# Kernel tuning notes

Measured on AMD Instinct MI355X. Metric: run time of the kernel, lower is better.

Reference implementation:

```python
import jax, jax.numpy as jnp
import numpy as np

N_NODES = 100000


def gcn_conv(x, edge_index, W, b):
    """PyG GCNConv: symmetric normalization with added self-loops.
    x: [N, Fin], edge_index: [2, E], W: [Fin, Fout], b: [Fout]
    """
    n = x.shape[0]
    h = x @ W  # [N, Fout] dense transform first (standard GCNConv order)
    loops = jnp.arange(n, dtype=edge_index.dtype)
    src = jnp.concatenate([edge_index[0], loops])  # self-loops appended
    dst = jnp.concatenate([edge_index[1], loops])
    deg = jax.ops.segment_sum(jnp.ones_like(dst, dtype=h.dtype), dst, num_segments=n)
    dinv = jax.lax.rsqrt(deg)  # deg >= 1 thanks to self-loops
    norm = dinv[src] * dinv[dst]  # [E+N]
    msgs = h[src] * norm[:, None]  # gather + scale
    out = jax.ops.segment_sum(msgs, dst, num_segments=n)  # scatter-add
    return out + b


def setup_inputs() -> dict:
    key = jax.random.key(0)
    k = jax.random.split(key, 9)
    in_c, hid, out_c = 128, 128, 64
    n_edges = 1600000
    x = jax.random.normal(k[0], (N_NODES, in_c), dtype=jnp.float32)
    edge_index = jax.random.randint(k[1], (2, n_edges), 0, N_NODES, dtype=jnp.int64)
    def lin(kw, kb, fan_in, fan_out):
        bound = 1.0 / np.sqrt(fan_in)
        W = jax.random.uniform(kw, (fan_in, fan_out), jnp.float32, -bound, bound)
        b = jax.random.uniform(kb, (fan_out,), jnp.float32, -bound, bound)
        return W, b
    W1, b1 = lin(k[2], k[3], in_c, hid)
    W2, b2 = lin(k[4], k[5], hid, hid)
    Wf, bf = lin(k[6], k[7], hid, out_c)
    return {"x": x, "edge_index": edge_index, "W1": W1, "b1": b1,
            "W2": W2, "b2": b2, "Wf": Wf, "bf": bf}


def reference(x, edge_index, W1, b1, W2, b2, Wf, bf):
    h = jax.nn.relu(gcn_conv(x, edge_index, W1, b1))
    h = jax.nn.relu(gcn_conv(h, edge_index, W2, b2))
    return h @ Wf + bf
```

## Files before the change

### kernel.cpp

```cpp
#include <hip/hip_runtime.h>
#include <stdint.h>

typedef short short8 __attribute__((ext_vector_type(8)));
typedef float floatx4 __attribute__((ext_vector_type(4)));

#define BK 256

static __device__ __forceinline__ float bflo(unsigned int u) {
    union { unsigned int i; float f; } v; v.i = u << 16; return v.f;
}
static __device__ __forceinline__ float bfhi(unsigned int u) {
    union { unsigned int i; float f; } v; v.i = u & 0xffff0000u; return v.f;
}
static __device__ __forceinline__ unsigned short f2bf(float f) {
    union { float f; unsigned int i; } v; v.f = f;
    unsigned int u = v.i;
    unsigned int r = u + 0x7fffu + ((u >> 16) & 1u);
    return (unsigned short)(r >> 16);
}


__global__ void k_zero_cnt(int* bucket_cnt, int K) {
    int i = blockIdx.x * 256 + threadIdx.x;
    if (i < K) bucket_cnt[i] = 0;
}

__global__ __launch_bounds__(256) void k_hist(const int* __restrict__ dst, int* bucket_cnt,
                                              int E, int N, int K) {
    __shared__ int h[512];
    int t = threadIdx.x;
    for (int i = t; i < K; i += 256) h[i] = 0;
    __syncthreads();
    int per = (E + gridDim.x - 1) / gridDim.x;
    int lo = blockIdx.x * per, hi = min(lo + per, E);
    for (int e = lo + t; e < hi; e += 256) {
        unsigned int d = (unsigned int)dst[e];
        if (d < (unsigned int)N) atomicAdd(&h[d >> 8], 1);
    }
    __syncthreads();
    for (int i = t; i < K; i += 256) if (h[i]) atomicAdd(&bucket_cnt[i], h[i]);
}

__global__ void k_scanK(const int* __restrict__ bucket_cnt, int* bucket_off, int* bucket_cur,
                        int* row_start, int K, int N) {
    __shared__ int s[512];
    int t = threadIdx.x;
    int v = (t < K) ? bucket_cnt[t] : 0;
    s[t] = v; __syncthreads();
    for (int off = 1; off < 512; off <<= 1) {
        int x = (t >= off) ? s[t - off] : 0;
        __syncthreads();
        s[t] += x;
        __syncthreads();
    }
    if (t < K) { bucket_off[t] = s[t] - v; bucket_cur[t] = s[t] - v; }
    if (t == K - 1) { bucket_off[K] = s[t]; row_start[N] = s[t]; }
}

__global__ __launch_bounds__(256) void k_binscatter(const int* __restrict__ src,
                                                    const int* __restrict__ dst,
                                                    int* bucket_cur, uint2* __restrict__ tmp,
                                                    int E, int N, int K) {
    __shared__ int h[512];
    __shared__ int base[512];
    int t = threadIdx.x;
    for (int i = t; i < K; i += 256) h[i] = 0;
    __syncthreads();
    int per = (E + gridDim.x - 1) / gridDim.x;
    int lo = blockIdx.x * per, hi = min(lo + per, E);
    for (int e = lo + t; e < hi; e += 256) {
        unsigned int d = (unsigned int)dst[e], sv = (unsigned int)src[e];
        if (d < (unsigned int)N && sv < (unsigned int)N) atomicAdd(&h[d >> 8], 1);
    }
    __syncthreads();
    for (int i = t; i < K; i += 256) {
        int c = h[i];
        base[i] = c ? atomicAdd(&bucket_cur[i], c) : 0;
        h[i] = 0;
    }
    __syncthreads();
    for (int e = lo + t; e < hi; e += 256) {
        unsigned int d = (unsigned int)dst[e], sv = (unsigned int)src[e];
        if (d < (unsigned int)N && sv < (unsigned int)N) {
            int k = d >> 8;
            int p = base[k] + atomicAdd(&h[k], 1);
            tmp[p] = make_uint2(sv, d);
        }
    }
}

__global__ __launch_bounds__(256) void k_fine(const uint2* __restrict__ tmp,
                                              const int* __restrict__ bucket_off,
                                              int* __restrict__ row_start, float* __restrict__ dinv,
                                              int* __restrict__ csr, int N) {
    __shared__ int deg[BK];
    __shared__ int scn[BK];
    __shared__ int cur[BK];
    int b = blockIdx.x;
    int t = threadIdx.x;
    int lo = bucket_off[b], hi = bucket_off[b + 1];
    deg[t] = 0;
    __syncthreads();
    for (int e = lo + t; e < hi; e += 256) {
        int d = tmp[e].y & (BK - 1);
        atomicAdd(&deg[d], 1);
    }
    __syncthreads();
    int v = deg[t];
    scn[t] = v; __syncthreads();
    for (int off = 1; off < 256; off <<= 1) {
        int x = (t >= off) ? scn[t - off] : 0;
        __syncthreads();
        scn[t] += x;
        __syncthreads();
    }
    int rs = lo + scn[t] - v;
    cur[t] = rs;
    int node = b * BK + t;
    if (node < N) { row_start[node] = rs; dinv[node] = rsqrtf((float)(v + 1)); }
    __syncthreads();
    for (int e = lo + t; e < hi; e += 256) {
        uint2 ed = tmp[e];
        int d = ed.y & (BK - 1);
        int p = atomicAdd(&cur[d], 1);
        csr[p] = (int)ed.x;
    }
}


template <int NOUT, bool SCALE, bool BIAS, bool XF32, bool OUTF32>
__global__ __launch_bounds__(256, 2) void k_gemm(
    const void* __restrict__ Xv, const float* __restrict__ W,
    const float* __restrict__ bias, const float* __restrict__ dinv,
    void* __restrict__ outv, int M) {
    __shared__ __align__(16) unsigned short Wl[NOUT * 136];
    int t = threadIdx.x;
    for (int idx = t; idx < 128 * NOUT; idx += 256) {
        int k = idx / NOUT, n = idx % NOUT;
        Wl[n * 136 + k] = f2bf(W[idx]);
    }
    __syncthreads();

    int wave = t >> 6, lane = t & 63;
    int quad = lane >> 4, l16 = lane & 15;
    int m0 = blockIdx.x * 64 + wave * 16;
    int mr = m0 + l16;
    int mrc = mr < M ? mr : M - 1;

    constexpr int NT = NOUT / 16;
    floatx4 acc[NT];
#pragma unroll
    for (int i = 0; i < NT; i++) acc[i] = (floatx4){0.f, 0.f, 0.f, 0.f};

#pragma unroll
    for (int kc = 0; kc < 4; kc++) {
        short8 a;
        if (XF32) {
            const float* X = (const float*)Xv;
            const float* p = X + (size_t)mrc * 128 + kc * 32 + quad * 8;
            float4 xa = *(const float4*)p;
            float4 xb = *(const float4*)(p + 4);
            a[0] = (short)f2bf(xa.x); a[1] = (short)f2bf(xa.y);
            a[2] = (short)f2bf(xa.z); a[3] = (short)f2bf(xa.w);
            a[4] = (short)f2bf(xb.x); a[5] = (short)f2bf(xb.y);
            a[6] = (short)f2bf(xb.z); a[7] = (short)f2bf(xb.w);
        } else {
            const unsigned short* X = (const unsigned short*)Xv;
            a = *(const short8*)(X + (size_t)mrc * 128 + kc * 32 + quad * 8);
        }
#pragma unroll
        for (int nt = 0; nt < NT; nt++) {
            short8 b = *(const short8*)(&Wl[(nt * 16 + l16) * 136 + kc * 32 + quad * 8]);
            acc[nt] = __builtin_amdgcn_mfma_f32_16x16x32_bf16(a, b, acc[nt], 0, 0, 0);
        }
    }

#pragma unroll
    for (int i = 0; i < 4; i++) {
        int r = m0 + quad * 4 + i;
        if (r >= M) continue;
        float sc = SCALE ? dinv[r] : 1.0f;
#pragma unroll
        for (int nt = 0; nt < NT; nt++) {
            int n = nt * 16 + l16;
            float v = acc[nt][i] * sc;
            if (BIAS) v += bias[n];
            if (OUTF32) {
                ((float*)outv)[(size_t)r * NOUT + n] = v;
            } else {
                ((unsigned short*)outv)[(size_t)r * NOUT + n] = f2bf(v);
            }
        }
    }
}


__global__ __launch_bounds__(256, 4) void k_aggregate(
    const unsigned short* __restrict__ Hs, const int* __restrict__ csr,
    const int* __restrict__ row_start,
    const float* __restrict__ dinv, const float* __restrict__ bias,
    unsigned short* __restrict__ out, int N, int E) {
    int wave = threadIdx.x >> 6, lane = threadIdx.x & 63;
    int node = blockIdx.x * 4 + wave;
    if (node >= N) return;
    int ch = lane * 2;
    int Nm1 = N - 1;

    unsigned int u = *(const unsigned int*)(Hs + (size_t)node * 128 + ch);
    float a0 = bflo(u), a1 = bfhi(u);

    int start = row_start[node];
    int end = row_start[node + 1];
    if (start < 0) start = 0;
    if (end > E) end = E;
    int e = start;
    for (; e + 4 <= end; e += 4) {
        int s0 = min(max(csr[e], 0), Nm1);
        int s1 = min(max(csr[e + 1], 0), Nm1);
        int s2 = min(max(csr[e + 2], 0), Nm1);
        int s3 = min(max(csr[e + 3], 0), Nm1);
        unsigned int u0 = *(const unsigned int*)(Hs + (size_t)s0 * 128 + ch);
        unsigned int u1 = *(const unsigned int*)(Hs + (size_t)s1 * 128 + ch);
        unsigned int u2 = *(const unsigned int*)(Hs + (size_t)s2 * 128 + ch);
        unsigned int u3 = *(const unsigned int*)(Hs + (size_t)s3 * 128 + ch);
        a0 += bflo(u0) + bflo(u1) + bflo(u2) + bflo(u3);
        a1 += bfhi(u0) + bfhi(u1) + bfhi(u2) + bfhi(u3);
    }
    for (; e < end; e++) {
        int s0 = min(max(csr[e], 0), Nm1);
        unsigned int u0 = *(const unsigned int*)(Hs + (size_t)s0 * 128 + ch);
        a0 += bflo(u0);
        a1 += bfhi(u0);
    }

    float di = dinv[node];
    float r0 = fmaxf(fmaf(di, a0, bias[ch]), 0.f);
    float r1 = fmaxf(fmaf(di, a1, bias[ch + 1]), 0.f);
    unsigned int pk = (unsigned int)f2bf(r0) | ((unsigned int)f2bf(r1) << 16);
    *(unsigned int*)(out + (size_t)node * 128 + ch) = pk;
}


extern "C" void kernel_launch(void* const* d_in, const int* in_sizes, int n_in,
                              void* d_out, int out_size, void* d_ws, size_t ws_size,
                              hipStream_t stream) {
    const float* x  = (const float*)d_in[0];
    const int* ei   = (const int*)d_in[1];
    const float* W1 = (const float*)d_in[2];
    const float* b1 = (const float*)d_in[3];
    const float* W2 = (const float*)d_in[4];
    const float* b2 = (const float*)d_in[5];
    const float* Wf = (const float*)d_in[6];
    const float* bf = (const float*)d_in[7];

    int N = in_sizes[0] / 128;
    int E = in_sizes[1] / 2;
    const int* src = ei;
    const int* dst = ei + E;
    int K = (N + BK - 1) / BK;

    size_t need = 0;
    auto pad = [](size_t b) { return (b + 255) & ~(size_t)255; };
    size_t o_bcnt = need; need += pad(512 * 4);
    size_t o_boff = need; need += pad(513 * 4);
    size_t o_bcur = need; need += pad(512 * 4);
    size_t o_rs   = need; need += pad(((size_t)N + 1) * 4);
    size_t o_dinv = need; need += pad((size_t)N * 4);
    size_t o_csr  = need; need += pad((size_t)E * 4);
    size_t o_hs   = need; need += pad((size_t)N * 128 * 2);
    size_t o_a    = need; need += pad((size_t)N * 128 * 2);
    if (ws_size < need) return;
    if ((size_t)E * 8 > (size_t)N * 128 * 2) return;

    char* ws = (char*)d_ws;
    int* bucket_cnt = (int*)(ws + o_bcnt);
    int* bucket_off = (int*)(ws + o_boff);
    int* bucket_cur = (int*)(ws + o_bcur);
    int* row_start  = (int*)(ws + o_rs);
    float* dinv     = (float*)(ws + o_dinv);
    int* csr        = (int*)(ws + o_csr);
    unsigned short* Hs = (unsigned short*)(ws + o_hs);
    unsigned short* A  = (unsigned short*)(ws + o_a);
    uint2* tmp      = (uint2*)A;

    k_zero_cnt<<<(K + 255) / 256, 256, 0, stream>>>(bucket_cnt, K);
    k_hist<<<256, 256, 0, stream>>>(dst, bucket_cnt, E, N, K);
    k_scanK<<<1, 512, 0, stream>>>(bucket_cnt, bucket_off, bucket_cur, row_start, K, N);
    k_binscatter<<<256, 256, 0, stream>>>(src, dst, bucket_cur, tmp, E, N, K);
    k_fine<<<K, 256, 0, stream>>>(tmp, bucket_off, row_start, dinv, csr, N);

    int GB = (N + 63) / 64;
    k_gemm<128, true, false, true, false><<<GB, 256, 0, stream>>>(x, W1, nullptr, dinv, Hs, N);
    k_aggregate<<<(N + 3) / 4, 256, 0, stream>>>(Hs, csr, row_start, dinv, b1, A, N, E);
    k_gemm<128, true, false, false, false><<<GB, 256, 0, stream>>>(A, W2, nullptr, dinv, Hs, N);
    k_aggregate<<<(N + 3) / 4, 256, 0, stream>>>(Hs, csr, row_start, dinv, b2, A, N, E);
    k_gemm<64, false, true, false, true><<<GB, 256, 0, stream>>>(A, Wf, bf, nullptr, d_out, N);
}
```

Before: 356.6 us.

## Slice feature matrices into 16-channel planes for cache-local gather aggregation

Hidden features are stored as eight 16-channel slices of [N,16] bf16, and aggregation runs one slice per block, so each slice (about 3.2MB) can stay resident in L2 during the random neighbor gathers. Within a wave, eight lanes cooperate on each of eight edges, and the partial sums are combined with cross-lane shuffles. Weights are converted to transposed bf16 once up front instead of in every GEMM block, and the GEMM grid is halved with a grid-stride loop so the weight tile is reused across two row blocks. In exchange there are more blocks, each doing narrower 32-byte gathers, plus extra shuffle reductions per node.

```diff
diff --git a/kernel.cpp b/kernel.cpp
--- a/kernel.cpp
+++ b/kernel.cpp
@@ -128,116 +128,138 @@
 }
 
 
-template <int NOUT, bool SCALE, bool BIAS, bool XF32, bool OUTF32>
+__global__ void k_wconv(const float* __restrict__ W, unsigned short* __restrict__ Wt,
+                        int K, int Nc) {
+    int i = blockIdx.x * 256 + threadIdx.x;
+    if (i < K * Nc) {
+        int k = i / Nc, n = i % Nc;
+        Wt[n * K + k] = f2bf(W[i]);
+    }
+}
+
+
+template <int NOUT, bool SCALE, bool BIAS, bool XF32, bool ASLICED, bool OSLICED>
 __global__ __launch_bounds__(256, 2) void k_gemm(
-    const void* __restrict__ Xv, const float* __restrict__ W,
+    const void* __restrict__ Xv, const unsigned short* __restrict__ Wbf,
     const float* __restrict__ bias, const float* __restrict__ dinv,
-    void* __restrict__ outv, int M) {
+    void* __restrict__ outv, int M, int MB) {
     __shared__ __align__(16) unsigned short Wl[NOUT * 136];
     int t = threadIdx.x;
-    for (int idx = t; idx < 128 * NOUT; idx += 256) {
-        int k = idx / NOUT, n = idx % NOUT;
-        Wl[n * 136 + k] = f2bf(W[idx]);
+    for (int c = t; c < NOUT * 16; c += 256) {
+        short8 v = *(const short8*)(Wbf + (size_t)c * 8);
+        *(short8*)(&Wl[(c >> 4) * 136 + (c & 15) * 8]) = v;
     }
     __syncthreads();
 
     int wave = t >> 6, lane = t & 63;
     int quad = lane >> 4, l16 = lane & 15;
-    int m0 = blockIdx.x * 64 + wave * 16;
-    int mr = m0 + l16;
-    int mrc = mr < M ? mr : M - 1;
-
     constexpr int NT = NOUT / 16;
-    floatx4 acc[NT];
-#pragma unroll
-    for (int i = 0; i < NT; i++) acc[i] = (floatx4){0.f, 0.f, 0.f, 0.f};
-
-#pragma unroll
-    for (int kc = 0; kc < 4; kc++) {
-        short8 a;
-        if (XF32) {
-            const float* X = (const float*)Xv;
-            const float* p = X + (size_t)mrc * 128 + kc * 32 + quad * 8;
-            float4 xa = *(const float4*)p;
-            float4 xb = *(const float4*)(p + 4);
-            a[0] = (short)f2bf(xa.x); a[1] = (short)f2bf(xa.y);
-            a[2] = (short)f2bf(xa.z); a[3] = (short)f2bf(xa.w);
-            a[4] = (short)f2bf(xb.x); a[5] = (short)f2bf(xb.y);
-            a[6] = (short)f2bf(xb.z); a[7] = (short)f2bf(xb.w);
-        } else {
-            const unsigned short* X = (const unsigned short*)Xv;
-            a = *(const short8*)(X + (size_t)mrc * 128 + kc * 32 + quad * 8);
-        }
-#pragma unroll
-        for (int nt = 0; nt < NT; nt++) {
-            short8 b = *(const short8*)(&Wl[(nt * 16 + l16) * 136 + kc * 32 + quad * 8]);
-            acc[nt] = __builtin_amdgcn_mfma_f32_16x16x32_bf16(a, b, acc[nt], 0, 0, 0);
-        }
-    }
-
-#pragma unroll
-    for (int i = 0; i < 4; i++) {
-        int r = m0 + quad * 4 + i;
-        if (r >= M) continue;
-        float sc = SCALE ? dinv[r] : 1.0f;
-#pragma unroll
-        for (int nt = 0; nt < NT; nt++) {
-            int n = nt * 16 + l16;
-            float v = acc[nt][i] * sc;
-            if (BIAS) v += bias[n];
-            if (OUTF32) {
-                ((float*)outv)[(size_t)r * NOUT + n] = v;
+
+    for (int mb = blockIdx.x; mb < MB; mb += gridDim.x) {
+        int m0 = mb * 64 + wave * 16;
+        int mr = m0 + l16;
+        int mrc = mr < M ? mr : M - 1;
+
+        floatx4 acc[NT];
+#pragma unroll
+        for (int i = 0; i < NT; i++) acc[i] = (floatx4){0.f, 0.f, 0.f, 0.f};
+
+#pragma unroll
+        for (int kc = 0; kc < 4; kc++) {
+            short8 a;
+            if (XF32) {
+                const float* X = (const float*)Xv;
+                const float* p = X + (size_t)mrc * 128 + kc * 32 + quad * 8;
+                float4 xa = *(const float4*)p;
+                float4 xb = *(const float4*)(p + 4);
+                a[0] = (short)f2bf(xa.x); a[1] = (short)f2bf(xa.y);
+                a[2] = (short)f2bf(xa.z); a[3] = (short)f2bf(xa.w);
+                a[4] = (short)f2bf(xb.x); a[5] = (short)f2bf(xb.y);
+                a[6] = (short)f2bf(xb.z); a[7] = (short)f2bf(xb.w);
+            } else if (ASLICED) {
+                const unsigned short* X = (const unsigned short*)Xv;
+                int slice = kc * 2 + (quad >> 1);
+                a = *(const short8*)(X + ((size_t)slice * M + mrc) * 16 + (quad & 1) * 8);
             } else {
-                ((unsigned short*)outv)[(size_t)r * NOUT + n] = f2bf(v);
+                const unsigned short* X = (const unsigned short*)Xv;
+                a = *(const short8*)(X + (size_t)mrc * 128 + kc * 32 + quad * 8);
             }
-        }
-    }
-}
-
-
-__global__ __launch_bounds__(256, 4) void k_aggregate(
-    const unsigned short* __restrict__ Hs, const int* __restrict__ csr,
-    const int* __restrict__ row_start,
-    const float* __restrict__ dinv, const float* __restrict__ bias,
-    unsigned short* __restrict__ out, int N, int E) {
+#pragma unroll
+            for (int nt = 0; nt < NT; nt++) {
+                short8 b = *(const short8*)(&Wl[(nt * 16 + l16) * 136 + kc * 32 + quad * 8]);
+                acc[nt] = __builtin_amdgcn_mfma_f32_16x16x32_bf16(a, b, acc[nt], 0, 0, 0);
+            }
+        }
+
+#pragma unroll
+        for (int i = 0; i < 4; i++) {
+            int r = m0 + quad * 4 + i;
+            if (r >= M) continue;
+            float sc = SCALE ? dinv[r] : 1.0f;
+#pragma unroll
+            for (int nt = 0; nt < NT; nt++) {
+                int n = nt * 16 + l16;
+                float v = acc[nt][i] * sc;
+                if (BIAS) v += bias[n];
+                if (OSLICED) {
+                    ((unsigned short*)outv)[((size_t)nt * M + r) * 16 + l16] = f2bf(v);
+                } else {
+                    ((float*)outv)[(size_t)r * NOUT + n] = v;
+                }
+            }
+        }
+    }
+}
+
+
+__global__ __launch_bounds__(256, 8) void k_agg_sliced(
+    const unsigned short* __restrict__ Hst, const int* __restrict__ csr,
+    const int* __restrict__ row_start, const float* __restrict__ dinv,
+    const float* __restrict__ bias, unsigned short* __restrict__ At, int N) {
+    int b = blockIdx.x;
+    int s = b & 7;
+    int nb = b >> 3;
     int wave = threadIdx.x >> 6, lane = threadIdx.x & 63;
-    int node = blockIdx.x * 4 + wave;
-    if (node >= N) return;
-    int ch = lane * 2;
+    int eg = lane >> 3, cp = lane & 7;
     int Nm1 = N - 1;
-
-    unsigned int u = *(const unsigned int*)(Hs + (size_t)node * 128 + ch);
-    float a0 = bflo(u), a1 = bfhi(u);
-
-    int start = row_start[node];
-    int end = row_start[node + 1];
-    if (start < 0) start = 0;
-    if (end > E) end = E;
-    int e = start;
-    for (; e + 4 <= end; e += 4) {
-        int s0 = min(max(csr[e], 0), Nm1);
-        int s1 = min(max(csr[e + 1], 0), Nm1);
-        int s2 = min(max(csr[e + 2], 0), Nm1);
-        int s3 = min(max(csr[e + 3], 0), Nm1);
-        unsigned int u0 = *(const unsigned int*)(Hs + (size_t)s0 * 128 + ch);
-        unsigned int u1 = *(const unsigned int*)(Hs + (size_t)s1 * 128 + ch);
-        unsigned int u2 = *(const unsigned int*)(Hs + (size_t)s2 * 128 + ch);
-        unsigned int u3 = *(const unsigned int*)(Hs + (size_t)s3 * 128 + ch);
-        a0 += bflo(u0) + bflo(u1) + bflo(u2) + bflo(u3);
-        a1 += bfhi(u0) + bfhi(u1) + bfhi(u2) + bfhi(u3);
-    }
-    for (; e < end; e++) {
-        int s0 = min(max(csr[e], 0), Nm1);
-        unsigned int u0 = *(const unsigned int*)(Hs + (size_t)s0 * 128 + ch);
-        a0 += bflo(u0);
-        a1 += bfhi(u0);
-    }
-
-    float di = dinv[node];
-    float r0 = fmaxf(fmaf(di, a0, bias[ch]), 0.f);
-    float r1 = fmaxf(fmaf(di, a1, bias[ch + 1]), 0.f);
-    unsigned int pk = (unsigned int)f2bf(r0) | ((unsigned int)f2bf(r1) << 16);
-    *(unsigned int*)(out + (size_t)node * 128 + ch) = pk;
+    const unsigned short* Ts = Hst + (size_t)s * N * 16;
+    unsigned short* As = At + (size_t)s * N * 16;
+    float bs0 = bias[s * 16 + cp * 2];
+    float bs1 = bias[s * 16 + cp * 2 + 1];
+
+    int node0 = nb * 64 + wave * 16;
+#pragma unroll 1
+    for (int ni = 0; ni < 16; ni++) {
+        int node = node0 + ni;
+        if (node >= N) break;
+        int start = row_start[node];
+        int end = row_start[node + 1];
+        float a0 = 0.f, a1 = 0.f;
+        int G = (end - start + 7) >> 3;
+        int e = start + eg;
+        for (int g = 0; g < G; g++, e += 8) {
+            int ec = e < end ? e : end - 1;
+            int id = __builtin_nontemporal_load(csr + ec);
+            id = min(max(id, 0), Nm1);
+            unsigned int u = *(const unsigned int*)(Ts + (size_t)id * 16 + cp * 2);
+            if (e < end) { a0 += bflo(u); a1 += bfhi(u); }
+        }
+#pragma unroll
+        for (int off = 8; off < 64; off <<= 1) {
+            a0 += __shfl_xor(a0, off);
+            a1 += __shfl_xor(a1, off);
+        }
+        unsigned int su = *(const unsigned int*)(Ts + (size_t)node * 16 + cp * 2);
+        a0 += bflo(su);
+        a1 += bfhi(su);
+        float di = dinv[node];
+        float r0 = fmaxf(fmaf(di, a0, bs0), 0.f);
+        float r1 = fmaxf(fmaf(di, a1, bs1), 0.f);
+        if (eg == 0) {
+            unsigned int pk = (unsigned int)f2bf(r0) | ((unsigned int)f2bf(r1) << 16);
+            __builtin_nontemporal_store(pk, (unsigned int*)(As + (size_t)node * 16 + cp * 2));
+        }
+    }
 }
 
 
@@ -266,6 +288,7 @@
     size_t o_bcur = need; need += pad(512 * 4);
     size_t o_rs   = need; need += pad(((size_t)N + 1) * 4);
     size_t o_dinv = need; need += pad((size_t)N * 4);
+    size_t o_wbf  = need; need += pad((16384 + 16384 + 8192) * 2);
     size_t o_csr  = need; need += pad((size_t)E * 4);
     size_t o_hs   = need; need += pad((size_t)N * 128 * 2);
     size_t o_a    = need; need += pad((size_t)N * 128 * 2);
@@ -278,10 +301,17 @@
     int* bucket_cur = (int*)(ws + o_bcur);
     int* row_start  = (int*)(ws + o_rs);
     float* dinv     = (float*)(ws + o_dinv);
+    unsigned short* wb1 = (unsigned short*)(ws + o_wbf);
+    unsigned short* wb2 = wb1 + 16384;
+    unsigned short* wbf = wb2 + 16384;
     int* csr        = (int*)(ws + o_csr);
-    unsigned short* Hs = (unsigned short*)(ws + o_hs);
-    unsigned short* A  = (unsigned short*)(ws + o_a);
-    uint2* tmp      = (uint2*)A;
+    unsigned short* Hst = (unsigned short*)(ws + o_hs);
+    unsigned short* At  = (unsigned short*)(ws + o_a);
+    uint2* tmp      = (uint2*)At;
+
+    k_wconv<<<64, 256, 0, stream>>>(W1, wb1, 128, 128);
+    k_wconv<<<64, 256, 0, stream>>>(W2, wb2, 128, 128);
+    k_wconv<<<32, 256, 0, stream>>>(Wf, wbf, 128, 64);
 
     k_zero_cnt<<<(K + 255) / 256, 256, 0, stream>>>(bucket_cnt, K);
     k_hist<<<256, 256, 0, stream>>>(dst, bucket_cnt, E, N, K);
@@ -289,10 +319,13 @@
     k_binscatter<<<256, 256, 0, stream>>>(src, dst, bucket_cur, tmp, E, N, K);
     k_fine<<<K, 256, 0, stream>>>(tmp, bucket_off, row_start, dinv, csr, N);
 
-    int GB = (N + 63) / 64;
-    k_gemm<128, true, false, true, false><<<GB, 256, 0, stream>>>(x, W1, nullptr, dinv, Hs, N);
-    k_aggregate<<<(N + 3) / 4, 256, 0, stream>>>(Hs, csr, row_start, dinv, b1, A, N, E);
-    k_gemm<128, true, false, false, false><<<GB, 256, 0, stream>>>(A, W2, nullptr, dinv, Hs, N);
-    k_aggregate<<<(N + 3) / 4, 256, 0, stream>>>(Hs, csr, row_start, dinv, b2, A, N, E);
-    k_gemm<64, false, true, false, true><<<GB, 256, 0, stream>>>(A, Wf, bf, nullptr, d_out, N);
-}
+    int MB = (N + 63) / 64;
+    int GG = (MB + 1) / 2;
+    int GA = 8 * ((N + 63) / 64);
+
+    k_gemm<128, true, false, true, false, true><<<GG, 256, 0, stream>>>(x, wb1, nullptr, dinv, Hst, N, MB);
+    k_agg_sliced<<<GA, 256, 0, stream>>>(Hst, csr, row_start, dinv, b1, At, N);
+    k_gemm<128, true, false, false, true, true><<<GG, 256, 0, stream>>>(At, wb2, nullptr, dinv, Hst, N, MB);
+    k_agg_sliced<<<GA, 256, 0, stream>>>(Hst, csr, row_start, dinv, b2, At, N);
+    k_gemm<64, false, true, false, true, false><<<GG, 256, 0, stream>>>(At, wbf, bf, nullptr, d_out, N, MB);
+}
```

Measured after the change: 867.2 us. +143.2%, slower.
